# Kernel optimization log

Measured on AMD Instinct MI355X. Metric: run time of the kernel, lower is better.

## Reference

```python
import math
import jax, jax.numpy as jnp
import numpy as np

DIM = 1024
NUM_HEADS = 16
HEAD_DIM = DIM // NUM_HEADS


def setup_inputs() -> dict:
    key = jax.random.key(0)
    ks = jax.random.split(key, 5)
    b, t, d = 2, 2048, DIM
    x = jax.random.normal(ks[0], (b, t, d), dtype=jnp.float32)
    mask = jnp.ones((b, t), dtype=jnp.float32)  # 1 = keep, 0 = pad
    s_in = 1.0 / math.sqrt(d)
    w_qkv = jax.random.normal(ks[1], (3 * d, d), dtype=jnp.float32) * s_in
    b_qkv = jnp.zeros((3 * d,), dtype=jnp.float32)
    w_out = jax.random.normal(ks[2], (d, d), dtype=jnp.float32) * s_in
    b_out = jnp.zeros((d,), dtype=jnp.float32)
    return {"x": x, "mask": mask, "w_qkv": w_qkv, "b_qkv": b_qkv,
            "w_out": w_out, "b_out": b_out}


def reference(x, mask, w_qkv, b_qkv, w_out, b_out):
    b, t, d = x.shape
    h, hd = NUM_HEADS, HEAD_DIM
    # qkv projection (torch Linear: x @ W^T + b)
    qkv = x @ w_qkv.T + b_qkv                          # [b,t,3d]
    q, k, v = jnp.split(qkv, 3, axis=-1)
    def reshape(z):
        return z.reshape(b, t, h, hd).transpose(0, 2, 1, 3)  # [b,h,t,hd]
    q, k, v = reshape(q), reshape(k), reshape(v)
    att = jnp.einsum('bhqd,bhkd->bhqk', q, k) / math.sqrt(hd)  # [b,h,t,t]
    causal = jnp.tril(jnp.ones((t, t), dtype=bool))            # [t,t]
    keep = causal[None, None, :, :] & (mask[:, None, None, :] != 0)
    att = jnp.where(keep, att, -jnp.inf)
    att = jax.nn.softmax(att, axis=-1)
    out = jnp.einsum('bhqk,bhkd->bhqd', att, v)        # [b,h,t,hd]
    out = out.transpose(0, 2, 1, 3).reshape(b, t, d)
    return out @ w_out.T + b_out
```

## Files before the change

kernel.cpp:

```cpp
#include <hip/hip_runtime.h>
#include <cmath>

#define B_ 2
#define T_ 2048
#define D_ 1024
#define H_ 16
#define HD_ 64
#define M_ (B_ * T_)
#define N3_ (3 * D_)
#define K_ 1024

typedef _Float16 halfx8 __attribute__((ext_vector_type(8)));
typedef _Float16 halfx4 __attribute__((ext_vector_type(4)));
typedef _Float16 halfx2 __attribute__((ext_vector_type(2)));
typedef __fp16 fp16x2 __attribute__((ext_vector_type(2)));
typedef float f32x4 __attribute__((ext_vector_type(4)));
typedef float f32x16 __attribute__((ext_vector_type(16)));

#define ASYNC_COPY16(gp, lp) \
  __builtin_amdgcn_global_load_lds((__attribute__((address_space(1))) void*)(gp), \
      (__attribute__((address_space(3))) void*)(lp), 16, 0, 0)

#define QSCALE 0.1803368801111204f
#define RTHR 4.0f

__device__ __forceinline__ float exp2fast(float x) {
#if __has_builtin(__builtin_amdgcn_exp2f)
    return __builtin_amdgcn_exp2f(x);
#else
    return exp2f(x);
#endif
}

__global__ __launch_bounds__(256) void prep_all(
    const float* __restrict__ x, const float* __restrict__ wq,
    const float* __restrict__ wo, const float* __restrict__ mask,
    _Float16* __restrict__ xh, _Float16* __restrict__ wqh,
    _Float16* __restrict__ woh, float* __restrict__ kbias,
    int* __restrict__ tflags)
{
    int bid = blockIdx.x;
    if (bid >= 4096) {
        int i = (bid - 4096) * 256 + threadIdx.x;
        float mv = mask[i];
        kbias[i] = (mv != 0.f) ? 0.f : -INFINITY;
        unsigned long long bal = __ballot(mv != 0.f);
        if ((threadIdx.x & 63) == 0) tflags[i >> 6] = (bal == ~0ULL) ? 1 : 0;
        return;
    }
    const float* s; _Float16* d; int off;
    if (bid < 2048)      { s = x;  d = xh;  off = bid; }
    else if (bid < 3584) { s = wq; d = wqh; off = bid - 2048; }
    else                 { s = wo; d = woh; off = bid - 3584; }
    int i = (off * 256 + threadIdx.x) * 8;
    float4 a = *(const float4*)(s + i);
    float4 b = *(const float4*)(s + i + 4);
    halfx8 h;
    h[0] = (_Float16)a.x; h[1] = (_Float16)a.y; h[2] = (_Float16)a.z; h[3] = (_Float16)a.w;
    h[4] = (_Float16)b.x; h[5] = (_Float16)b.y; h[6] = (_Float16)b.z; h[7] = (_Float16)b.w;
    *(halfx8*)(d + i) = h;
}

__global__ __launch_bounds__(256) void gemm_qkv(
    const _Float16* __restrict__ A, const _Float16* __restrict__ Wt,
    const float* __restrict__ bias,
    _Float16* __restrict__ qh, _Float16* __restrict__ kh, _Float16* __restrict__ vth)
{
    __shared__ _Float16 As[128 * 32];
    __shared__ _Float16 Bs[128 * 32];
    const int tid = threadIdx.x;
    const int lane = tid & 63, w = tid >> 6;
    const int col = lane & 15, quad = lane >> 4;
    const int wr = w >> 1, wc = w & 1;
    const int m0 = blockIdx.y << 7, n0 = blockIdx.x << 7;

    const int c0 = w * 2, c1 = c0 + 1;
    const int r0 = c0 * 16 + (lane >> 2), r1 = c1 * 16 + (lane >> 2);
    const int ks = (lane & 3) << 3;

    f32x4 acc[4][4] = {};

    for (int k0 = 0; k0 < K_; k0 += 32) {
        ASYNC_COPY16(A  + (size_t)(m0 + r0) * K_ + k0 + ks, &As[c0 * 512]);
        ASYNC_COPY16(A  + (size_t)(m0 + r1) * K_ + k0 + ks, &As[c1 * 512]);
        ASYNC_COPY16(Wt + (size_t)(n0 + r0) * K_ + k0 + ks, &Bs[c0 * 512]);
        ASYNC_COPY16(Wt + (size_t)(n0 + r1) * K_ + k0 + ks, &Bs[c1 * 512]);
        __syncthreads();
        halfx8 af[4], bf[4];
#pragma unroll
        for (int i = 0; i < 4; ++i)
            af[i] = *(const halfx8*)&As[(wr * 64 + i * 16 + col) * 32 + quad * 8];
#pragma unroll
        for (int j = 0; j < 4; ++j)
            bf[j] = *(const halfx8*)&Bs[(wc * 64 + j * 16 + col) * 32 + quad * 8];
#pragma unroll
        for (int i = 0; i < 4; ++i)
#pragma unroll
            for (int j = 0; j < 4; ++j)
                acc[i][j] = __builtin_amdgcn_mfma_f32_16x16x32_f16(af[i], bf[j], acc[i][j], 0, 0, 0);
        __syncthreads();
    }

#pragma unroll
    for (int i = 0; i < 4; ++i) {
#pragma unroll
        for (int r = 0; r < 4; ++r) {
            int m = m0 + wr * 64 + i * 16 + quad * 4 + r;
            int bb = m >> 11, tt = m & (T_ - 1);
#pragma unroll
            for (int j = 0; j < 4; ++j) {
                int n = n0 + wc * 64 + j * 16 + col;
                float val = acc[i][j][r] + bias[n];
                int which = n >> 10, head = (n >> 6) & 15, dd = n & 63;
                if (which == 0) {
                    qh[((size_t)(bb * H_ + head) * T_ + tt) * HD_ + dd] = (_Float16)(val * QSCALE);
                } else if (which == 1) {
                    int hi = ((dd >> 3) ^ (tt & 7) ^ ((tt >> 3) & 7)) & 7;
                    int dds = (hi << 3) | (dd & 7);
                    kh[((size_t)(bb * H_ + head) * T_ + tt) * HD_ + dds] = (_Float16)val;
                } else {
                    int hi = (((tt >> 3) & 7) ^ (dd & 7) ^ ((dd >> 3) & 7)) & 7;
                    int tts = (tt & ~63) | (hi << 3) | (tt & 7);
                    vth[((size_t)(bb * H_ + head) * HD_ + dd) * T_ + tts] = (_Float16)val;
                }
            }
        }
    }
}

__global__ __launch_bounds__(256) void gemm_out(
    const _Float16* __restrict__ A, const _Float16* __restrict__ Wt,
    const float* __restrict__ bias, float* __restrict__ C)
{
    __shared__ _Float16 As[128 * 32];
    __shared__ _Float16 Bs[64 * 32];
    const int tid = threadIdx.x;
    const int lane = tid & 63, w = tid >> 6;
    const int col = lane & 15, quad = lane >> 4;
    const int m0 = blockIdx.y << 7, n0 = blockIdx.x << 6;

    const int c0 = w * 2, c1 = c0 + 1;
    const int rA0 = c0 * 16 + (lane >> 2), rA1 = c1 * 16 + (lane >> 2);
    const int rB = w * 16 + (lane >> 2);
    const int ks = (lane & 3) << 3;

    f32x4 acc[2][4] = {};

    for (int k0 = 0; k0 < K_; k0 += 32) {
        ASYNC_COPY16(A  + (size_t)(m0 + rA0) * K_ + k0 + ks, &As[c0 * 512]);
        ASYNC_COPY16(A  + (size_t)(m0 + rA1) * K_ + k0 + ks, &As[c1 * 512]);
        ASYNC_COPY16(Wt + (size_t)(n0 + rB) * K_ + k0 + ks, &Bs[w * 512]);
        __syncthreads();
        halfx8 af[2], bf[4];
#pragma unroll
        for (int i = 0; i < 2; ++i)
            af[i] = *(const halfx8*)&As[(w * 32 + i * 16 + col) * 32 + quad * 8];
#pragma unroll
        for (int j = 0; j < 4; ++j)
            bf[j] = *(const halfx8*)&Bs[(j * 16 + col) * 32 + quad * 8];
#pragma unroll
        for (int i = 0; i < 2; ++i)
#pragma unroll
            for (int j = 0; j < 4; ++j)
                acc[i][j] = __builtin_amdgcn_mfma_f32_16x16x32_f16(af[i], bf[j], acc[i][j], 0, 0, 0);
        __syncthreads();
    }

#pragma unroll
    for (int i = 0; i < 2; ++i) {
#pragma unroll
        for (int r = 0; r < 4; ++r) {
            int m = m0 + w * 32 + i * 16 + quad * 4 + r;
#pragma unroll
            for (int j = 0; j < 4; ++j) {
                int n = n0 + j * 16 + col;
                C[(size_t)m * D_ + n] = acc[i][j][r] + bias[n];
            }
        }
    }
}

__global__ __launch_bounds__(256, 3) void attn_kernel(
    const _Float16* __restrict__ qh, const _Float16* __restrict__ kh,
    const _Float16* __restrict__ vth, const float* __restrict__ kbias,
    const int* __restrict__ tflags,
    _Float16* __restrict__ oh)
{
    __shared__ _Float16 Ks[2][64 * 64];
    __shared__ _Float16 Vt[2][64 * 64];

    const int bid = blockIdx.x;
    const int qt = 15 - (bid >> 5);
    const int hb = bid & 31;
    const int h = hb & 15, b = hb >> 4;
    const int tid = threadIdx.x;
    const int lane = tid & 63, w = tid >> 6;
    const int l31 = lane & 31, q2 = lane >> 5;

    const int kt0 = 0;
    const int ktend = 2 * qt + 1;

    const int bh = b * H_ + h;
    const _Float16* qp = qh + (size_t)bh * T_ * HD_;
    const _Float16* kp = kh + (size_t)bh * T_ * HD_;
    const _Float16* vp = vth + (size_t)bh * HD_ * T_;
    const float* kb = kbias + (size_t)b * T_;
    const int* tf = tflags + b * 32;

    const int qbase = qt * 128 + w * 32;
    const int q_row = qbase + l31;

    halfx8 bq[4];
#pragma unroll
    for (int hc = 0; hc < 4; ++hc)
        bq[hc] = *(const halfx8*)(qp + (size_t)q_row * HD_ + hc * 16 + q2 * 8);

    float mrow = -INFINITY;
    float lrow = 0.f;
    f32x16 oacc[2] = {};
    const fp16x2 one2 = {(__fp16)1.f, (__fp16)1.f};

    {
        const _Float16* ksrc = kp + (size_t)(kt0 * 64 + w * 16) * HD_;
        ASYNC_COPY16(ksrc + lane * 8, &Ks[0][(w * 16) * 64]);
        ASYNC_COPY16(ksrc + 8 * HD_ + lane * 8, &Ks[0][(w * 16 + 8) * 64]);
        const _Float16* vsrc = vp + (size_t)(w * 16 + (lane >> 3)) * T_
                                 + kt0 * 64 + (lane & 7) * 8;
        ASYNC_COPY16(vsrc, &Vt[0][(w * 16) * 64]);
        ASYNC_COPY16(vsrc + 8 * T_, &Vt[0][(w * 16 + 8) * 64]);
    }

    for (int kt = kt0; kt <= ktend; ++kt) {
        const int cur = (kt - kt0) & 1;
        __syncthreads();
        if (kt < ktend) {
            const int nb = cur ^ 1;
            const _Float16* ksrc = kp + (size_t)((kt + 1) * 64 + w * 16) * HD_;
            ASYNC_COPY16(ksrc + lane * 8, &Ks[nb][(w * 16) * 64]);
            ASYNC_COPY16(ksrc + 8 * HD_ + lane * 8, &Ks[nb][(w * 16 + 8) * 64]);
            const _Float16* vsrc = vp + (size_t)(w * 16 + (lane >> 3)) * T_
                                     + (kt + 1) * 64 + (lane & 7) * 8;
            ASYNC_COPY16(vsrc, &Vt[nb][(w * 16) * 64]);
            ASYNC_COPY16(vsrc + 8 * T_, &Vt[nb][(w * 16 + 8) * 64]);
        }
        if (kt * 64 > qbase + 31) continue;

        const int allkeep = tf[kt];
        const int kb2max = (qbase + 31 - kt * 64 >= 32) ? 2 : 1;

        auto qk_half = [&](int kb2v) -> f32x16 {
            f32x16 a = {};
#pragma unroll
            for (int hc = 0; hc < 4; ++hc) {
                int seg = (hc * 2 + q2) ^ (l31 & 7) ^ ((kb2v * 4 + (l31 >> 3)) & 7);
                halfx8 ka = *(const halfx8*)&Ks[cur][(kb2v * 32 + l31) * 64 + seg * 8];
                a = __builtin_amdgcn_mfma_f32_32x32x16_f16(ka, bq[hc], a, 0, 0, 0);
            }
            return a;
        };
        f32x16 sa0, sa1;
        __builtin_amdgcn_s_setprio(1);
        sa0 = qk_half(0);
        if (kb2max == 2) sa1 = qk_half(1);
        __builtin_amdgcn_s_setprio(0);

        auto smpv = [&](const f32x16& a, int kb2v) {
            float t0 = fmaxf(fmaxf(a[0],  a[1]),  a[2]);
            float t1 = fmaxf(fmaxf(a[3],  a[4]),  a[5]);
            float t2 = fmaxf(fmaxf(a[6],  a[7]),  a[8]);
            float t3 = fmaxf(fmaxf(a[9],  a[10]), a[11]);
            float t4 = fmaxf(fmaxf(a[12], a[13]), a[14]);
            float u0 = fmaxf(fmaxf(t0, t1), t2);
            float u1 = fmaxf(fmaxf(t3, t4), a[15]);
            float mx = fmaxf(u0, u1);

            if (__any(mx > mrow + RTHR)) {
                float mxo = fmaxf(mx, __shfl_xor(mx, 32, 64));
                float mnew = fmaxf(mrow, mxo);
                float alpha = exp2fast(mrow - mnew);
                lrow *= alpha;
#pragma unroll
                for (int db = 0; db < 2; ++db)
#pragma unroll
                    for (int r = 0; r < 16; ++r) oacc[db][r] *= alpha;
                mrow = mnew;
            }

            const bool fastk = allkeep && (kt * 64 + kb2v * 32 + 31 <= qbase);
            halfx4 pf[4];
            float s0 = 0.f, s1 = 0.f;
            if (fastk) {
#pragma unroll
                for (int cc = 0; cc < 4; ++cc) {
                    float e0 = exp2fast(a[cc * 4 + 0] - mrow);
                    float e1 = exp2fast(a[cc * 4 + 1] - mrow);
                    float e2 = exp2fast(a[cc * 4 + 2] - mrow);
                    float e3 = exp2fast(a[cc * 4 + 3] - mrow);
                    fp16x2 lo = __builtin_amdgcn_cvt_pkrtz(e0, e1);
                    fp16x2 hi = __builtin_amdgcn_cvt_pkrtz(e2, e3);
                    halfx2* pfv = (halfx2*)&pf[cc];
                    pfv[0] = __builtin_bit_cast(halfx2, lo);
                    pfv[1] = __builtin_bit_cast(halfx2, hi);
#if __has_builtin(__builtin_amdgcn_fdot2)
                    s0 = __builtin_amdgcn_fdot2(lo, one2, s0, false);
                    s1 = __builtin_amdgcn_fdot2(hi, one2, s1, false);
#else
                    s0 += e0 + e1; s1 += e2 + e3;
#endif
                }
            } else {
#pragma unroll
                for (int cc = 0; cc < 4; ++cc) {
                    float e[4];
#pragma unroll
                    for (int j = 0; j < 4; ++j) {
                        int key = kt * 64 + kb2v * 32 + 8 * cc + 4 * q2 + j;
                        float add = allkeep ? 0.f : kb[key];
                        e[j] = (key <= q_row) ? exp2fast(a[cc * 4 + j] + add - mrow) : 0.f;
                    }
                    fp16x2 lo = __builtin_amdgcn_cvt_pkrtz(e[0], e[1]);
                    fp16x2 hi = __builtin_amdgcn_cvt_pkrtz(e[2], e[3]);
                    halfx2* pfv = (halfx2*)&pf[cc];
                    pfv[0] = __builtin_bit_cast(halfx2, lo);
                    pfv[1] = __builtin_bit_cast(halfx2, hi);
#if __has_builtin(__builtin_amdgcn_fdot2)
                    s0 = __builtin_amdgcn_fdot2(lo, one2, s0, false);
                    s1 = __builtin_amdgcn_fdot2(hi, one2, s1, false);
#else
                    s0 += e[0] + e[1]; s1 += e[2] + e[3];
#endif
                }
            }
            lrow += s0 + s1;

            __builtin_amdgcn_s_setprio(1);
#pragma unroll
            for (int db = 0; db < 2; ++db)
#pragma unroll
                for (int cc = 0; cc < 4; ++cc) {
                    int ck = kb2v * 4 + cc;
                    int seg = ck ^ (l31 & 7) ^ ((db * 4 + (l31 >> 3)) & 7);
                    halfx4 va = *(const halfx4*)&Vt[cur][(db * 32 + l31) * 64 + seg * 8 + q2 * 4];
                    oacc[db] = __builtin_amdgcn_mfma_f32_32x32x8f16(va, pf[cc], oacc[db], 0, 0, 0);
                }
            __builtin_amdgcn_s_setprio(0);
        };

        smpv(sa0, 0);
        if (kb2max == 2) smpv(sa1, 1);
    }

    lrow += __shfl_xor(lrow, 32, 64);
    const float linv = 1.f / lrow;

    const int qloc = w * 32 + l31;
    _Float16* pob = oh + ((size_t)(b * T_ + qt * 128 + qloc)) * D_ + h * 64;
#pragma unroll
    for (int db = 0; db < 2; ++db)
#pragma unroll
        for (int gg = 0; gg < 4; ++gg) {
            halfx4 ov;
#pragma unroll
            for (int j = 0; j < 4; ++j)
                ov[j] = (_Float16)(oacc[db][gg * 4 + j] * linv);
            *(halfx4*)(pob + db * 32 + 8 * gg + 4 * q2) = ov;
        }
}

extern "C" void kernel_launch(void* const* d_in, const int* in_sizes, int n_in,
                              void* d_out, int out_size, void* d_ws, size_t ws_size,
                              hipStream_t stream)
{
    (void)in_sizes; (void)n_in; (void)out_size; (void)ws_size;
    const float* x     = (const float*)d_in[0];
    const float* mask  = (const float*)d_in[1];
    const float* w_qkv = (const float*)d_in[2];
    const float* b_qkv = (const float*)d_in[3];
    const float* w_out = (const float*)d_in[4];
    const float* b_out = (const float*)d_in[5];
    float* out = (float*)d_out;

    const size_t QKV1 = (size_t)B_ * H_ * T_ * HD_;
    _Float16* xh  = (_Float16*)d_ws;
    _Float16* wqh = xh  + (size_t)M_ * K_;
    _Float16* woh = wqh + (size_t)N3_ * K_;
    _Float16* qh  = woh + (size_t)D_ * K_;
    _Float16* kh  = qh  + QKV1;
    _Float16* vth = kh  + QKV1;
    _Float16* oh  = vth + QKV1;
    float* kbias  = (float*)(oh + QKV1);
    int* tflags   = (int*)(kbias + (size_t)B_ * T_);

    prep_all<<<4112, 256, 0, stream>>>(x, w_qkv, w_out, mask,
                                       xh, wqh, woh, kbias, tflags);
    gemm_qkv<<<dim3(N3_ / 128, M_ / 128), 256, 0, stream>>>(
        xh, wqh, b_qkv, qh, kh, vth);
    attn_kernel<<<dim3(512, 1, 1), 256, 0, stream>>>(
        qh, kh, vth, kbias, tflags, oh);
    gemm_out<<<dim3(D_ / 64, M_ / 128), 256, 0, stream>>>(
        oh, woh, b_out, out);
}
```

Measured before the change: 193.4 us.

## Split long causal attention query tiles across two blocks with combine kernel

Query tiles 8-15 have their key range split into two halves, each handled by a separate block. Each block writes an unnormalized partial output plus its row max and row sum, and a new combine kernel merges the pairs with log-sum-exp weighting. A lookup table orders the work items so the longest pieces start first. The goal is better load balance and more blocks for the causal workload, at the cost of an extra launch, extra global traffic for the partials, and fp16 storage of unnormalized accumulators.

```diff
diff --git a/kernel.cpp b/kernel.cpp
--- a/kernel.cpp
+++ b/kernel.cpp
@@ -31,6 +31,9 @@
     return exp2f(x);
 #endif
 }
+
+__device__ const int QT2_OF[24] = {15,15,7, 14,14, 13,13,6, 12,12, 11,11,5, 10,10, 9,9,4, 8,8, 3,2,1,0};
+__device__ const int C2_OF[24]  = { 0, 1,0,  0, 1,  0, 1,0,  0, 1,  0, 1,0,  0, 1, 0,1,0,  0,1, 0,0,0,0};
 
 __global__ __launch_bounds__(256) void prep_all(
     const float* __restrict__ x, const float* __restrict__ wq,
@@ -184,21 +187,23 @@
     const _Float16* __restrict__ qh, const _Float16* __restrict__ kh,
     const _Float16* __restrict__ vth, const float* __restrict__ kbias,
     const int* __restrict__ tflags,
-    _Float16* __restrict__ oh)
+    float* __restrict__ pm, float* __restrict__ pl,
+    _Float16* __restrict__ po, _Float16* __restrict__ oh)
 {
     __shared__ _Float16 Ks[2][64 * 64];
     __shared__ _Float16 Vt[2][64 * 64];
 
-    const int bid = blockIdx.x;
-    const int qt = 15 - (bid >> 5);
-    const int hb = bid & 31;
+    const int item = blockIdx.x >> 5;
+    const int qt = QT2_OF[item], c = C2_OF[item];
+    const int hb = blockIdx.x & 31;
     const int h = hb & 15, b = hb >> 4;
+    const bool split = (qt >= 8);
     const int tid = threadIdx.x;
     const int lane = tid & 63, w = tid >> 6;
     const int l31 = lane & 31, q2 = lane >> 5;
 
-    const int kt0 = 0;
-    const int ktend = 2 * qt + 1;
+    const int kt0 = (split && c) ? (qt + 1) : 0;
+    const int ktend = (split && !c) ? qt : (2 * qt + 1);
 
     const int bh = b * H_ + h;
     const _Float16* qp = qh + (size_t)bh * T_ * HD_;
@@ -351,20 +356,74 @@
     }
 
     lrow += __shfl_xor(lrow, 32, 64);
-    const float linv = 1.f / lrow;
 
     const int qloc = w * 32 + l31;
-    _Float16* pob = oh + ((size_t)(b * T_ + qt * 128 + qloc)) * D_ + h * 64;
-#pragma unroll
-    for (int db = 0; db < 2; ++db)
-#pragma unroll
-        for (int gg = 0; gg < 4; ++gg) {
-            halfx4 ov;
-#pragma unroll
-            for (int j = 0; j < 4; ++j)
-                ov[j] = (_Float16)(oacc[db][gg * 4 + j] * linv);
-            *(halfx4*)(pob + db * 32 + 8 * gg + 4 * q2) = ov;
+    _Float16* ohrow = oh + ((size_t)(b * T_ + qt * 128 + qloc)) * D_ + h * 64;
+
+    if (!split) {
+        const float linv = 1.f / lrow;
+#pragma unroll
+        for (int db = 0; db < 2; ++db)
+#pragma unroll
+            for (int gg = 0; gg < 4; ++gg) {
+                halfx4 ov;
+#pragma unroll
+                for (int j = 0; j < 4; ++j)
+                    ov[j] = (_Float16)(oacc[db][gg * 4 + j] * linv);
+                *(halfx4*)(ohrow + db * 32 + 8 * gg + 4 * q2) = ov;
+            }
+    } else {
+        const int slot = (bh * 8 + (qt - 8)) * 2 + c;
+        if (q2 == 0) {
+            pm[(size_t)slot * 128 + qloc] = mrow;
+            pl[(size_t)slot * 128 + qloc] = lrow;
         }
+        _Float16* pob = (c == 0) ? ohrow
+                      : po + ((size_t)(bh * 8 + (qt - 8)) * 128 + qloc) * 64;
+#pragma unroll
+        for (int db = 0; db < 2; ++db)
+#pragma unroll
+            for (int gg = 0; gg < 4; ++gg) {
+                halfx4 ov;
+#pragma unroll
+                for (int j = 0; j < 4; ++j)
+                    ov[j] = (_Float16)(oacc[db][gg * 4 + j]);
+                *(halfx4*)(pob + db * 32 + 8 * gg + 4 * q2) = ov;
+            }
+    }
+}
+
+__global__ __launch_bounds__(256) void attn_combine(
+    const float* __restrict__ pm, const float* __restrict__ pl,
+    const _Float16* __restrict__ po, _Float16* __restrict__ oh)
+{
+    const int qi = blockIdx.x;
+    const int h = blockIdx.y, b = blockIdx.z;
+    const int bh = b * H_ + h;
+    const int tid = threadIdx.x;
+    const int r = tid >> 1, dh = tid & 1;
+
+    const int s0 = (bh * 8 + qi) * 2;
+    float m0 = pm[(size_t)s0 * 128 + r],       m1 = pm[(size_t)(s0 + 1) * 128 + r];
+    float l0 = pl[(size_t)s0 * 128 + r],       l1 = pl[(size_t)(s0 + 1) * 128 + r];
+    float ms = fmaxf(m0, m1);
+    float w0 = exp2f(m0 - ms), w1 = exp2f(m1 - ms);
+    float linv = 1.f / (w0 * l0 + w1 * l1);
+    w0 *= linv; w1 *= linv;
+
+    _Float16* ohrow = oh + ((size_t)(b * T_ + (qi + 8) * 128 + r)) * D_ + h * 64 + dh * 32;
+    const _Float16* src = po + ((size_t)(bh * 8 + qi) * 128 + r) * 64 + dh * 32;
+
+#pragma unroll
+    for (int g = 0; g < 4; ++g) {
+        halfx8 o0 = *(const halfx8*)(ohrow + g * 8);
+        halfx8 o1 = *(const halfx8*)(src + g * 8);
+        halfx8 ov;
+#pragma unroll
+        for (int j = 0; j < 8; ++j)
+            ov[j] = (_Float16)(w0 * (float)o0[j] + w1 * (float)o1[j]);
+        *(halfx8*)(ohrow + g * 8) = ov;
+    }
 }
 
 extern "C" void kernel_launch(void* const* d_in, const int* in_sizes, int n_in,
@@ -388,15 +447,20 @@
     _Float16* kh  = qh  + QKV1;
     _Float16* vth = kh  + QKV1;
     _Float16* oh  = vth + QKV1;
-    float* kbias  = (float*)(oh + QKV1);
-    int* tflags   = (int*)(kbias + (size_t)B_ * T_);
+    _Float16* po  = oh  + QKV1;
+    float* kbias  = (float*)(po + (size_t)32 * 8 * 128 * 64);
+    float* pm     = kbias + (size_t)B_ * T_;
+    float* pl     = pm + (size_t)32 * 16 * 128;
+    int* tflags   = (int*)(pl + (size_t)32 * 16 * 128);
 
     prep_all<<<4112, 256, 0, stream>>>(x, w_qkv, w_out, mask,
                                        xh, wqh, woh, kbias, tflags);
     gemm_qkv<<<dim3(N3_ / 128, M_ / 128), 256, 0, stream>>>(
         xh, wqh, b_qkv, qh, kh, vth);
-    attn_kernel<<<dim3(512, 1, 1), 256, 0, stream>>>(
-        qh, kh, vth, kbias, tflags, oh);
+    attn_kernel<<<dim3(768, 1, 1), 256, 0, stream>>>(
+        qh, kh, vth, kbias, tflags, pm, pl, po, oh);
+    attn_combine<<<dim3(8, H_, B_), 256, 0, stream>>>(
+        pm, pl, po, oh);
     gemm_out<<<dim3(D_ / 64, M_ / 128), 256, 0, stream>>>(
         oh, woh, b_out, out);
 }
```

Measured after the change: 181.7 us. 6.1% less time.
